# Kernel tuning notes

Measured on AMD Instinct MI355X. Metric: run time of the kernel, lower is better.

## Reference

```python
import jax, jax.numpy as jnp
import numpy as np

NUM_HEADS = 16
SUBSET_SIZE = 256
NODES_PER_GRAPH = 4096
BATCH_SIZE = 128
NODE_DIM = 128
HEAD_DIM = 128
LN_EPS = 1e-5


def _layer_norm(x, w, b):
    mu = jnp.mean(x, axis=-1, keepdims=True)
    var = jnp.var(x, axis=-1, keepdims=True)
    return (x - mu) * jax.lax.rsqrt(var + LN_EPS) * w + b


def setup_inputs() -> dict:
    key = jax.random.key(0)
    k_emb, k_w1, k_w2 = jax.random.split(key, 3)
    rng = np.random.default_rng(0)
    # per-head random node subsets within a graph (irregular gather pattern)
    subsets = np.stack([rng.choice(NODES_PER_GRAPH, SUBSET_SIZE, replace=False)
                        for _ in range(NUM_HEADS)])  # [H, S]
    all_subset_nodes = jnp.asarray(subsets.reshape(-1), dtype=jnp.int32)  # [H*S]
    head_batch = jnp.repeat(jnp.arange(NUM_HEADS, dtype=jnp.int32), SUBSET_SIZE)
    n_total = BATCH_SIZE * NODES_PER_GRAPH
    node_embeddings = jax.random.normal(k_emb, (n_total, NODE_DIM), dtype=jnp.float32)
    batch = jnp.repeat(jnp.arange(BATCH_SIZE, dtype=jnp.int32), NODES_PER_GRAPH)
    d3 = NODE_DIM * 3
    proj1_weights = jax.random.normal(k_w1, (NUM_HEADS, d3, HEAD_DIM * 2), dtype=jnp.float32) / np.sqrt(d3)
    proj1_bias = jnp.zeros((NUM_HEADS, HEAD_DIM * 2), jnp.float32)
    proj2_weights = jax.random.normal(k_w2, (NUM_HEADS, HEAD_DIM * 2, HEAD_DIM), dtype=jnp.float32) / np.sqrt(HEAD_DIM * 2)
    proj2_bias = jnp.zeros((NUM_HEADS, HEAD_DIM), jnp.float32)
    return {
        'node_embeddings': node_embeddings,
        'proj1_weights': proj1_weights,
        'proj1_bias': proj1_bias,
        'norm1_weight': jnp.ones((HEAD_DIM * 2,), jnp.float32),
        'norm1_bias': jnp.zeros((HEAD_DIM * 2,), jnp.float32),
        'proj2_weights': proj2_weights,
        'proj2_bias': proj2_bias,
        'norm2_weight': jnp.ones((HEAD_DIM,), jnp.float32),
        'norm2_bias': jnp.zeros((HEAD_DIM,), jnp.float32),
        'batch': batch,
        'all_subset_nodes': all_subset_nodes,
        'head_batch': head_batch,
        'batch_size': BATCH_SIZE,
    }


def reference(node_embeddings, proj1_weights, proj1_bias, norm1_weight, norm1_bias,
              proj2_weights, proj2_bias, norm2_weight, norm2_bias,
              batch, all_subset_nodes, head_batch, batch_size):
    B = int(batch_size)
    H = proj1_weights.shape[0]
    D = node_embeddings.shape[1]
    S = all_subset_nodes.shape[0]  # total subset nodes per graph (H*subset_size)
    # per-graph node offsets from bincount/cumsum (mirrors torch path)
    nodes_per_graph = jnp.bincount(batch, length=B)
    graph_offsets = jnp.concatenate([jnp.zeros((1,), nodes_per_graph.dtype),
                                     jnp.cumsum(nodes_per_graph)[:-1]])
    flat_idx = (graph_offsets[:, None] + all_subset_nodes[None, :]).reshape(-1)  # [B*S]
    emb = node_embeddings[flat_idx]  # [B*S, D] irregular gather
    # combined (graph, head) segment id
    seg = (jnp.arange(B, dtype=head_batch.dtype)[:, None] * H + head_batch[None, :]).reshape(-1)
    num_seg = B * H
    sum_emb = jax.ops.segment_sum(emb, seg, num_segments=num_seg)          # [B*H, D]
    counts = jax.ops.segment_sum(jnp.ones((emb.shape[0],), emb.dtype), seg, num_segments=num_seg)
    mean_emb = sum_emb / jnp.maximum(counts, 1.0)[:, None]
    max_emb = jax.ops.segment_max(emb, seg, num_segments=num_seg)
    max_emb = jnp.where(counts[:, None] > 0, max_emb, 0.0)  # empty segments -> 0 (torch init)
    combined = jnp.concatenate([mean_emb, max_emb, sum_emb], axis=-1).reshape(B, H, 3 * D)
    h1 = jnp.einsum('bni,nij->bnj', combined, proj1_weights) + proj1_bias[None]
    h1 = jax.nn.relu(_layer_norm(h1, norm1_weight, norm1_bias))  # dropout p in eval -> identity
    out = jnp.einsum('bni,nij->bnj', h1, proj2_weights) + proj2_bias[None]
    out = jax.nn.relu(_layer_norm(out, norm2_weight, norm2_bias))
    return out  # [B, H, head_embed_dim]
```

## Files before the change

kernel.cpp:

```cpp
#include <hip/hip_runtime.h>
#include <hip/hip_bf16.h>
#include <math.h>

#define NH   16
#define SS   256
#define NPG  4096
#define NB   128
#define ND   128
#define D3   384
#define H2   256
#define HD   128
#define LNEPS 1e-5f
#define G    2

__global__ __launch_bounds__(256, 4)
void mhe_fused(const float* __restrict__ emb,
               const float* __restrict__ W1, const float* __restrict__ B1,
               const float* __restrict__ Gm1, const float* __restrict__ Bt1,
               const float* __restrict__ W2, const float* __restrict__ B2,
               const float* __restrict__ Gm2, const float* __restrict__ Bt2,
               const int*   __restrict__ subset,
               float* __restrict__ out)
{
    __shared__ int    s_nodes[SS];
    __shared__ float  s_psum[G][8][ND];
    __shared__ float  s_pmax[G][8][ND];
    __shared__ float  s_comb[G][D3];
    __shared__ float  s_h1[G][H2];
    __shared__ float4 s_part[4];

    const int tid  = threadIdx.x;
    const int lane = tid & 63;
    const int wid  = tid >> 6;

    int raw     = blockIdx.x;
    int logical = (raw & 7) * 128 + (raw >> 3);
    int h  = logical >> 6;
    int bp = logical & 63;
    int b0 = bp * 2, b1 = b0 + 1;

    s_nodes[tid] = subset[h * SS + tid];
    __syncthreads();

    const int c  = tid & 31;
    const int rp = tid >> 5;
    const float4* g0 = reinterpret_cast<const float4*>(emb) + (long)b0 * NPG * (ND / 4);
    const float4* g1 = reinterpret_cast<const float4*>(emb) + (long)b1 * NPG * (ND / 4);

    float4 s0 = make_float4(0.f, 0.f, 0.f, 0.f);
    float4 s1 = s0;
    float4 m0 = make_float4(-INFINITY, -INFINITY, -INFINITY, -INFINITY);
    float4 m1 = m0;

    #pragma unroll 1
    for (int r = rp; r < SS; r += 32) {
        int o0 = s_nodes[r]      * (ND / 4) + c;
        int o1 = s_nodes[r + 8]  * (ND / 4) + c;
        int o2 = s_nodes[r + 16] * (ND / 4) + c;
        int o3 = s_nodes[r + 24] * (ND / 4) + c;
        float4 a0 = g0[o0]; float4 a1 = g0[o1]; float4 a2 = g0[o2]; float4 a3 = g0[o3];
        float4 d0 = g1[o0]; float4 d1 = g1[o1]; float4 d2 = g1[o2]; float4 d3 = g1[o3];

        s0.x += (a0.x + a1.x) + (a2.x + a3.x);
        s0.y += (a0.y + a1.y) + (a2.y + a3.y);
        s0.z += (a0.z + a1.z) + (a2.z + a3.z);
        s0.w += (a0.w + a1.w) + (a2.w + a3.w);
        m0.x = fmaxf(m0.x, fmaxf(fmaxf(a0.x, a1.x), fmaxf(a2.x, a3.x)));
        m0.y = fmaxf(m0.y, fmaxf(fmaxf(a0.y, a1.y), fmaxf(a2.y, a3.y)));
        m0.z = fmaxf(m0.z, fmaxf(fmaxf(a0.z, a1.z), fmaxf(a2.z, a3.z)));
        m0.w = fmaxf(m0.w, fmaxf(fmaxf(a0.w, a1.w), fmaxf(a2.w, a3.w)));

        s1.x += (d0.x + d1.x) + (d2.x + d3.x);
        s1.y += (d0.y + d1.y) + (d2.y + d3.y);
        s1.z += (d0.z + d1.z) + (d2.z + d3.z);
        s1.w += (d0.w + d1.w) + (d2.w + d3.w);
        m1.x = fmaxf(m1.x, fmaxf(fmaxf(d0.x, d1.x), fmaxf(d2.x, d3.x)));
        m1.y = fmaxf(m1.y, fmaxf(fmaxf(d0.y, d1.y), fmaxf(d2.y, d3.y)));
        m1.z = fmaxf(m1.z, fmaxf(fmaxf(d0.z, d1.z), fmaxf(d2.z, d3.z)));
        m1.w = fmaxf(m1.w, fmaxf(fmaxf(d0.w, d1.w), fmaxf(d2.w, d3.w)));
    }
    *reinterpret_cast<float4*>(&s_psum[0][rp][4 * c]) = s0;
    *reinterpret_cast<float4*>(&s_pmax[0][rp][4 * c]) = m0;
    *reinterpret_cast<float4*>(&s_psum[1][rp][4 * c]) = s1;
    *reinterpret_cast<float4*>(&s_pmax[1][rp][4 * c]) = m1;
    __syncthreads();

    {
        int g = tid >> 7, j = tid & 127;
        float s = 0.f, m = -INFINITY;
        #pragma unroll
        for (int r2 = 0; r2 < 8; ++r2) {
            s += s_psum[g][r2][j];
            m = fmaxf(m, s_pmax[g][r2][j]);
        }
        s_comb[g][j]          = s * (1.f / SS);
        s_comb[g][ND + j]     = m;
        s_comb[g][2 * ND + j] = s;
    }
    __syncthreads();

    float h1a, h1b;
    {
        const float* w = W1 + (long)h * D3 * H2 + tid;
        float a0 = B1[h * H2 + tid];
        float a1 = a0;
        for (int i = 0; i < D3; i += 8) {
            float wv[8];
            #pragma unroll
            for (int j = 0; j < 8; ++j) wv[j] = w[(i + j) * H2];
            #pragma unroll
            for (int j = 0; j < 8; ++j) {
                a0 = fmaf(s_comb[0][i + j], wv[j], a0);
                a1 = fmaf(s_comb[1][i + j], wv[j], a1);
            }
        }
        float4 v = make_float4(a0, a0 * a0, a1, a1 * a1);
        #pragma unroll
        for (int off = 32; off >= 1; off >>= 1) {
            v.x += __shfl_xor(v.x, off);
            v.y += __shfl_xor(v.y, off);
            v.z += __shfl_xor(v.z, off);
            v.w += __shfl_xor(v.w, off);
        }
        if (lane == 0) s_part[wid] = v;
        __syncthreads();
        float4 t0 = s_part[0], t1 = s_part[1], t2 = s_part[2], t3 = s_part[3];
        float4 tot = make_float4(t0.x + t1.x + t2.x + t3.x, t0.y + t1.y + t2.y + t3.y,
                                 t0.z + t1.z + t2.z + t3.z, t0.w + t1.w + t2.w + t3.w);
        float mu0 = tot.x * (1.f / H2), var0 = tot.y * (1.f / H2) - mu0 * mu0;
        float mu1 = tot.z * (1.f / H2), var1 = tot.w * (1.f / H2) - mu1 * mu1;
        float gv = Gm1[tid], bv = Bt1[tid];
        h1a = fmaxf((a0 - mu0) * rsqrtf(var0 + LNEPS) * gv + bv, 0.f);
        h1b = fmaxf((a1 - mu1) * rsqrtf(var1 + LNEPS) * gv + bv, 0.f);
        s_h1[0][tid] = h1a;
        s_h1[1][tid] = h1b;
    }
    __syncthreads();

    float a0 = 0.f, a1 = 0.f;
    if (tid < HD) {
        const float* w = W2 + (long)h * H2 * HD + tid;
        a0 = B2[h * HD + tid];
        a1 = a0;
        for (int i = 0; i < H2; i += 8) {
            float wv[8];
            #pragma unroll
            for (int j = 0; j < 8; ++j) wv[j] = w[(i + j) * HD];
            #pragma unroll
            for (int j = 0; j < 8; ++j) {
                a0 = fmaf(s_h1[0][i + j], wv[j], a0);
                a1 = fmaf(s_h1[1][i + j], wv[j], a1);
            }
        }
    }
    {
        float4 v = (tid < HD) ? make_float4(a0, a0 * a0, a1, a1 * a1)
                              : make_float4(0.f, 0.f, 0.f, 0.f);
        #pragma unroll
        for (int off = 32; off >= 1; off >>= 1) {
            v.x += __shfl_xor(v.x, off);
            v.y += __shfl_xor(v.y, off);
            v.z += __shfl_xor(v.z, off);
            v.w += __shfl_xor(v.w, off);
        }
        if (lane == 0) s_part[wid] = v;
        __syncthreads();
        if (tid < HD) {
            float4 t0 = s_part[0], t1 = s_part[1], t2 = s_part[2], t3 = s_part[3];
            float4 tot = make_float4(t0.x + t1.x + t2.x + t3.x, t0.y + t1.y + t2.y + t3.y,
                                     t0.z + t1.z + t2.z + t3.z, t0.w + t1.w + t2.w + t3.w);
            float mu0 = tot.x * (1.f / HD), var0 = tot.y * (1.f / HD) - mu0 * mu0;
            float mu1 = tot.z * (1.f / HD), var1 = tot.w * (1.f / HD) - mu1 * mu1;
            float gv = Gm2[tid], bv = Bt2[tid];
            float v0 = fmaxf((a0 - mu0) * rsqrtf(var0 + LNEPS) * gv + bv, 0.f);
            float v1 = fmaxf((a1 - mu1) * rsqrtf(var1 + LNEPS) * gv + bv, 0.f);
            out[((long)b0 * NH + h) * HD + tid] = v0;
            out[((long)b1 * NH + h) * HD + tid] = v1;
        }
    }
}

extern "C" void kernel_launch(void* const* d_in, const int* in_sizes, int n_in,
                              void* d_out, int out_size, void* d_ws, size_t ws_size,
                              hipStream_t stream)
{
    const float* emb  = (const float*)d_in[0];
    const float* W1   = (const float*)d_in[1];
    const float* B1   = (const float*)d_in[2];
    const float* Gm1  = (const float*)d_in[3];
    const float* Bt1  = (const float*)d_in[4];
    const float* W2   = (const float*)d_in[5];
    const float* B2   = (const float*)d_in[6];
    const float* Gm2  = (const float*)d_in[7];
    const float* Bt2  = (const float*)d_in[8];
    const int* subset = (const int*)d_in[10];
    float* out = (float*)d_out;

    mhe_fused<<<dim3(NH * (NB / G)), dim3(256), 0, stream>>>(
        emb, W1, B1, Gm1, Bt1, W2, B2, Gm2, Bt2, subset, out);
}
```

Before: 390.1 us.

## Process four graphs per block with 512 threads to reuse head weights

Each block now handles four graphs for one head instead of two, with 512 threads. The gather loop loads four graphs per subset node, and the projection stages split the extra graphs across thread halves so every thread does useful work in the second MLP layer. This halves the number of blocks and the total reads of W1/W2 per head. In exchange it uses more shared memory (larger partial-sum buffers) and more registers per thread, which may lower occupancy.

```diff
diff --git a/kernel.cpp b/kernel.cpp
--- a/kernel.cpp
+++ b/kernel.cpp
@@ -11,9 +11,9 @@
 #define H2   256
 #define HD   128
 #define LNEPS 1e-5f
-#define G    2
+#define G4   4
 
-__global__ __launch_bounds__(256, 4)
+__global__ __launch_bounds__(512, 4)
 void mhe_fused(const float* __restrict__ emb,
                const float* __restrict__ W1, const float* __restrict__ B1,
                const float* __restrict__ Gm1, const float* __restrict__ Bt1,
@@ -23,73 +23,70 @@
                float* __restrict__ out)
 {
     __shared__ int    s_nodes[SS];
-    __shared__ float  s_psum[G][8][ND];
-    __shared__ float  s_pmax[G][8][ND];
-    __shared__ float  s_comb[G][D3];
-    __shared__ float  s_h1[G][H2];
-    __shared__ float4 s_part[4];
+    __shared__ float  s_psum[G4][16][ND];
+    __shared__ float  s_pmax[G4][16][ND];
+    __shared__ float  s_comb[G4][D3];
+    __shared__ float  s_h1[G4][H2];
+    __shared__ float4 s_part[8];
 
     const int tid  = threadIdx.x;
     const int lane = tid & 63;
     const int wid  = tid >> 6;
 
     int raw     = blockIdx.x;
-    int logical = (raw & 7) * 128 + (raw >> 3);
-    int h  = logical >> 6;
-    int bp = logical & 63;
-    int b0 = bp * 2, b1 = b0 + 1;
+    int logical = (raw & 7) * 64 + (raw >> 3);
+    int h = logical >> 5;
+    int q = logical & 31;
+    int b = q * 4;
 
-    s_nodes[tid] = subset[h * SS + tid];
+    if (tid < SS) s_nodes[tid] = subset[h * SS + tid];
     __syncthreads();
 
     const int c  = tid & 31;
     const int rp = tid >> 5;
-    const float4* g0 = reinterpret_cast<const float4*>(emb) + (long)b0 * NPG * (ND / 4);
-    const float4* g1 = reinterpret_cast<const float4*>(emb) + (long)b1 * NPG * (ND / 4);
+    const float4* eb = reinterpret_cast<const float4*>(emb);
+    long gb[G4];
+    #pragma unroll
+    for (int g = 0; g < G4; ++g) gb[g] = (long)(b + g) * NPG * (ND / 4);
 
-    float4 s0 = make_float4(0.f, 0.f, 0.f, 0.f);
-    float4 s1 = s0;
-    float4 m0 = make_float4(-INFINITY, -INFINITY, -INFINITY, -INFINITY);
-    float4 m1 = m0;
+    float4 sum[G4], mx[G4];
+    #pragma unroll
+    for (int g = 0; g < G4; ++g) {
+        sum[g] = make_float4(0.f, 0.f, 0.f, 0.f);
+        mx[g]  = make_float4(-INFINITY, -INFINITY, -INFINITY, -INFINITY);
+    }
 
     #pragma unroll 1
     for (int r = rp; r < SS; r += 32) {
-        int o0 = s_nodes[r]      * (ND / 4) + c;
-        int o1 = s_nodes[r + 8]  * (ND / 4) + c;
-        int o2 = s_nodes[r + 16] * (ND / 4) + c;
-        int o3 = s_nodes[r + 24] * (ND / 4) + c;
-        float4 a0 = g0[o0]; float4 a1 = g0[o1]; float4 a2 = g0[o2]; float4 a3 = g0[o3];
-        float4 d0 = g1[o0]; float4 d1 = g1[o1]; float4 d2 = g1[o2]; float4 d3 = g1[o3];
-
-        s0.x += (a0.x + a1.x) + (a2.x + a3.x);
-        s0.y += (a0.y + a1.y) + (a2.y + a3.y);
-        s0.z += (a0.z + a1.z) + (a2.z + a3.z);
-        s0.w += (a0.w + a1.w) + (a2.w + a3.w);
-        m0.x = fmaxf(m0.x, fmaxf(fmaxf(a0.x, a1.x), fmaxf(a2.x, a3.x)));
-        m0.y = fmaxf(m0.y, fmaxf(fmaxf(a0.y, a1.y), fmaxf(a2.y, a3.y)));
-        m0.z = fmaxf(m0.z, fmaxf(fmaxf(a0.z, a1.z), fmaxf(a2.z, a3.z)));
-        m0.w = fmaxf(m0.w, fmaxf(fmaxf(a0.w, a1.w), fmaxf(a2.w, a3.w)));
-
-        s1.x += (d0.x + d1.x) + (d2.x + d3.x);
-        s1.y += (d0.y + d1.y) + (d2.y + d3.y);
-        s1.z += (d0.z + d1.z) + (d2.z + d3.z);
-        s1.w += (d0.w + d1.w) + (d2.w + d3.w);
-        m1.x = fmaxf(m1.x, fmaxf(fmaxf(d0.x, d1.x), fmaxf(d2.x, d3.x)));
-        m1.y = fmaxf(m1.y, fmaxf(fmaxf(d0.y, d1.y), fmaxf(d2.y, d3.y)));
-        m1.z = fmaxf(m1.z, fmaxf(fmaxf(d0.z, d1.z), fmaxf(d2.z, d3.z)));
-        m1.w = fmaxf(m1.w, fmaxf(fmaxf(d0.w, d1.w), fmaxf(d2.w, d3.w)));
+        int n0 = s_nodes[r]      * (ND / 4) + c;
+        int n1 = s_nodes[r + 16] * (ND / 4) + c;
+        float4 v0[G4], v1[G4];
+        #pragma unroll
+        for (int g = 0; g < G4; ++g) { v0[g] = eb[gb[g] + n0]; v1[g] = eb[gb[g] + n1]; }
+        #pragma unroll
+        for (int g = 0; g < G4; ++g) {
+            sum[g].x += v0[g].x + v1[g].x;
+            sum[g].y += v0[g].y + v1[g].y;
+            sum[g].z += v0[g].z + v1[g].z;
+            sum[g].w += v0[g].w + v1[g].w;
+            mx[g].x = fmaxf(mx[g].x, fmaxf(v0[g].x, v1[g].x));
+            mx[g].y = fmaxf(mx[g].y, fmaxf(v0[g].y, v1[g].y));
+            mx[g].z = fmaxf(mx[g].z, fmaxf(v0[g].z, v1[g].z));
+            mx[g].w = fmaxf(mx[g].w, fmaxf(v0[g].w, v1[g].w));
+        }
     }
-    *reinterpret_cast<float4*>(&s_psum[0][rp][4 * c]) = s0;
-    *reinterpret_cast<float4*>(&s_pmax[0][rp][4 * c]) = m0;
-    *reinterpret_cast<float4*>(&s_psum[1][rp][4 * c]) = s1;
-    *reinterpret_cast<float4*>(&s_pmax[1][rp][4 * c]) = m1;
+    #pragma unroll
+    for (int g = 0; g < G4; ++g) {
+        *reinterpret_cast<float4*>(&s_psum[g][rp][4 * c]) = sum[g];
+        *reinterpret_cast<float4*>(&s_pmax[g][rp][4 * c]) = mx[g];
+    }
     __syncthreads();
 
     {
         int g = tid >> 7, j = tid & 127;
         float s = 0.f, m = -INFINITY;
         #pragma unroll
-        for (int r2 = 0; r2 < 8; ++r2) {
+        for (int r2 = 0; r2 < 16; ++r2) {
             s += s_psum[g][r2][j];
             m = fmaxf(m, s_pmax[g][r2][j]);
         }
@@ -99,10 +96,12 @@
     }
     __syncthreads();
 
-    float h1a, h1b;
     {
-        const float* w = W1 + (long)h * D3 * H2 + tid;
-        float a0 = B1[h * H2 + tid];
+        const int col = tid & 255;
+        const int gh  = tid >> 8;
+        const int gA  = 2 * gh, gB = 2 * gh + 1;
+        const float* w = W1 + (long)h * D3 * H2 + col;
+        float a0 = B1[h * H2 + col];
         float a1 = a0;
         for (int i = 0; i < D3; i += 8) {
             float wv[8];
@@ -110,8 +109,8 @@
             for (int j = 0; j < 8; ++j) wv[j] = w[(i + j) * H2];
             #pragma unroll
             for (int j = 0; j < 8; ++j) {
-                a0 = fmaf(s_comb[0][i + j], wv[j], a0);
-                a1 = fmaf(s_comb[1][i + j], wv[j], a1);
+                a0 = fmaf(s_comb[gA][i + j], wv[j], a0);
+                a1 = fmaf(s_comb[gB][i + j], wv[j], a1);
             }
         }
         float4 v = make_float4(a0, a0 * a0, a1, a1 * a1);
@@ -124,59 +123,45 @@
         }
         if (lane == 0) s_part[wid] = v;
         __syncthreads();
-        float4 t0 = s_part[0], t1 = s_part[1], t2 = s_part[2], t3 = s_part[3];
+        int base = gh * 4;
+        float4 t0 = s_part[base], t1 = s_part[base + 1],
+               t2 = s_part[base + 2], t3 = s_part[base + 3];
         float4 tot = make_float4(t0.x + t1.x + t2.x + t3.x, t0.y + t1.y + t2.y + t3.y,
                                  t0.z + t1.z + t2.z + t3.z, t0.w + t1.w + t2.w + t3.w);
         float mu0 = tot.x * (1.f / H2), var0 = tot.y * (1.f / H2) - mu0 * mu0;
         float mu1 = tot.z * (1.f / H2), var1 = tot.w * (1.f / H2) - mu1 * mu1;
-        float gv = Gm1[tid], bv = Bt1[tid];
-        h1a = fmaxf((a0 - mu0) * rsqrtf(var0 + LNEPS) * gv + bv, 0.f);
-        h1b = fmaxf((a1 - mu1) * rsqrtf(var1 + LNEPS) * gv + bv, 0.f);
-        s_h1[0][tid] = h1a;
-        s_h1[1][tid] = h1b;
+        float gv = Gm1[col], bv = Bt1[col];
+        s_h1[gA][col] = fmaxf((a0 - mu0) * rsqrtf(var0 + LNEPS) * gv + bv, 0.f);
+        s_h1[gB][col] = fmaxf((a1 - mu1) * rsqrtf(var1 + LNEPS) * gv + bv, 0.f);
     }
     __syncthreads();
 
-    float a0 = 0.f, a1 = 0.f;
-    if (tid < HD) {
-        const float* w = W2 + (long)h * H2 * HD + tid;
-        a0 = B2[h * HD + tid];
-        a1 = a0;
+    {
+        const int col = tid & 127;
+        const int g3  = tid >> 7;
+        const float* w = W2 + (long)h * H2 * HD + col;
+        float a = B2[h * HD + col];
         for (int i = 0; i < H2; i += 8) {
             float wv[8];
             #pragma unroll
             for (int j = 0; j < 8; ++j) wv[j] = w[(i + j) * HD];
             #pragma unroll
-            for (int j = 0; j < 8; ++j) {
-                a0 = fmaf(s_h1[0][i + j], wv[j], a0);
-                a1 = fmaf(s_h1[1][i + j], wv[j], a1);
-            }
+            for (int j = 0; j < 8; ++j) a = fmaf(s_h1[g3][i + j], wv[j], a);
         }
-    }
-    {
-        float4 v = (tid < HD) ? make_float4(a0, a0 * a0, a1, a1 * a1)
-                              : make_float4(0.f, 0.f, 0.f, 0.f);
+        float2 v = make_float2(a, a * a);
         #pragma unroll
         for (int off = 32; off >= 1; off >>= 1) {
             v.x += __shfl_xor(v.x, off);
             v.y += __shfl_xor(v.y, off);
-            v.z += __shfl_xor(v.z, off);
-            v.w += __shfl_xor(v.w, off);
         }
-        if (lane == 0) s_part[wid] = v;
+        if (lane == 0) s_part[wid] = make_float4(v.x, v.y, 0.f, 0.f);
         __syncthreads();
-        if (tid < HD) {
-            float4 t0 = s_part[0], t1 = s_part[1], t2 = s_part[2], t3 = s_part[3];
-            float4 tot = make_float4(t0.x + t1.x + t2.x + t3.x, t0.y + t1.y + t2.y + t3.y,
-                                     t0.z + t1.z + t2.z + t3.z, t0.w + t1.w + t2.w + t3.w);
-            float mu0 = tot.x * (1.f / HD), var0 = tot.y * (1.f / HD) - mu0 * mu0;
-            float mu1 = tot.z * (1.f / HD), var1 = tot.w * (1.f / HD) - mu1 * mu1;
-            float gv = Gm2[tid], bv = Bt2[tid];
-            float v0 = fmaxf((a0 - mu0) * rsqrtf(var0 + LNEPS) * gv + bv, 0.f);
-            float v1 = fmaxf((a1 - mu1) * rsqrtf(var1 + LNEPS) * gv + bv, 0.f);
-            out[((long)b0 * NH + h) * HD + tid] = v0;
-            out[((long)b1 * NH + h) * HD + tid] = v1;
-        }
+        float4 p0 = s_part[2 * g3], p1 = s_part[2 * g3 + 1];
+        float sx = p0.x + p1.x, sxx = p0.y + p1.y;
+        float mu = sx * (1.f / HD), var = sxx * (1.f / HD) - mu * mu;
+        float gv = Gm2[col], bv = Bt2[col];
+        float o = fmaxf((a - mu) * rsqrtf(var + LNEPS) * gv + bv, 0.f);
+        out[((long)(b + g3) * NH + h) * HD + col] = o;
     }
 }
 
@@ -196,6 +181,6 @@
     const int* subset = (const int*)d_in[10];
     float* out = (float*)d_out;
 
-    mhe_fused<<<dim3(NH * (NB / G)), dim3(256), 0, stream>>>(
+    mhe_fused<<<dim3(NH * (NB / G4)), dim3(512), 0, stream>>>(
         emb, W1, B1, Gm1, Bt1, W2, B2, Gm2, Bt2, subset, out);
 }
```

Result: no change. 385.9 us (-1.1%).
